# Performance work log

Hardware: AMD Instinct MI355X
Metric: run time of the kernel (lower is better)

The kernel has to match this reference:

```python
import jax, jax.numpy as jnp
import numpy as np

D_MODEL = 1024
NUM_HEADS = 16
D_K = D_MODEL // NUM_HEADS
ROPE_BASE = 10000.0


def _rotate_half(x):
    # interleaved pairs: (x0, x1) -> (-x1, x0)
    x1 = x[..., ::2]
    x2 = x[..., 1::2]
    return jnp.stack((-x2, x1), axis=-1).reshape(x.shape)


def _rope(q, k):
    seq_len = q.shape[-2]
    freqs = ROPE_BASE ** (jnp.arange(0, D_K, 2, dtype=q.dtype) / D_K)  # [D_K/2]
    angles = jnp.arange(seq_len, dtype=q.dtype)[:, None] / freqs[None, :]  # [S, D_K/2]
    sin = jnp.repeat(jnp.sin(angles), 2, axis=-1)[None, None]  # [1,1,S,D_K]
    cos = jnp.repeat(jnp.cos(angles), 2, axis=-1)[None, None]
    return q * cos + _rotate_half(q) * sin, k * cos + _rotate_half(k) * sin


def setup_inputs() -> dict:
    key = jax.random.key(0)
    ks = jax.random.split(key, 9)
    B, S, D = 2, 2048, D_MODEL
    s = 1.0 / np.sqrt(D)
    inp = {
        "x": jax.random.normal(ks[0], (B, S, D), dtype=jnp.float32),
        "wq": jax.random.uniform(ks[1], (D, D), jnp.float32, -s, s),
        "bq": jax.random.uniform(ks[2], (D,), jnp.float32, -s, s),
        "wk": jax.random.uniform(ks[3], (D, D), jnp.float32, -s, s),
        "bk": jax.random.uniform(ks[4], (D,), jnp.float32, -s, s),
        "wv": jax.random.uniform(ks[5], (D, D), jnp.float32, -s, s),
        "bv": jax.random.uniform(ks[6], (D,), jnp.float32, -s, s),
        "wo": jax.random.uniform(ks[7], (D, D), jnp.float32, -s, s),
        "bo": jax.random.uniform(ks[8], (D,), jnp.float32, -s, s),
    }
    return inp


def reference(x, wq, bq, wk, bk, wv, bv, wo, bo):
    B, S, D = x.shape
    H, dk = NUM_HEADS, D_K
    # torch Linear: y = x @ W.T + b
    Q = (x @ wq.T + bq).reshape(B, S, H, dk).transpose(0, 2, 1, 3)  # [B,H,S,dk]
    K = (x @ wk.T + bk).reshape(B, S, H, dk).transpose(0, 2, 1, 3)
    V = (x @ wv.T + bv).reshape(B, S, H, dk).transpose(0, 2, 1, 3)
    Q, K = _rope(Q, K)
    score = jnp.einsum("bhqd,bhkd->bhqk", Q, K) / jnp.sqrt(jnp.asarray(dk, x.dtype))
    attn_w = jax.nn.softmax(score, axis=-1)
    out = jnp.einsum("bhqk,bhkd->bhqd", attn_w, V)  # [B,H,S,dk]
    out = out.transpose(0, 2, 1, 3).reshape(B, S, D)
    return out @ wo.T + bo
```

## Files before the change

### kernel.cpp

```cpp
#include <hip/hip_runtime.h>
#include <hip/hip_bf16.h>
#include <math.h>

typedef __bf16 bf16_t;
typedef __bf16 bf16x4_t __attribute__((ext_vector_type(4)));
typedef __bf16 bf16x8_t __attribute__((ext_vector_type(8)));
typedef float  f32x4_t  __attribute__((ext_vector_type(4)));

#define SEQ 2048
#define DM  1024
#define NH  16
#define DK  64
#define ROPE_C 0.4152410118609203f
#define EXP_C (1.4426950408889634f / 8.0f)

#define GLD16(gp, lp) \
  __builtin_amdgcn_global_load_lds((__attribute__((address_space(1))) const void*)(gp), \
                                   (__attribute__((address_space(3))) void*)(lp), 16, 0, 0)

__global__ __launch_bounds__(256)
void prep_kernel(const float* __restrict__ x,  const float* __restrict__ wq,
                 const float* __restrict__ wk, const float* __restrict__ wv,
                 const float* __restrict__ wo, bf16_t* __restrict__ dst,
                 float2* __restrict__ lut) {
  if (blockIdx.x < 8192) {
    int i = blockIdx.x * 256 + threadIdx.x;
    const float* s;
    if (i < 1048576) {
      s = x + (size_t)i * 4;
    } else {
      int j = i - 1048576;
      int w = j >> 18;
      const float* base = (w == 0) ? wq : (w == 1) ? wk : (w == 2) ? wv : wo;
      s = base + (size_t)(j & 262143) * 4;
    }
    float4 v = *(const float4*)s;
    bf16x4_t o;
    o.x = (bf16_t)v.x; o.y = (bf16_t)v.y; o.z = (bf16_t)v.z; o.w = (bf16_t)v.w;
    ((bf16x4_t*)dst)[i] = o;
  } else {
    int i = (blockIdx.x - 8192) * 256 + threadIdx.x;
    int s = i >> 5, f = i & 31;
    float ang = (float)s * exp2f(-ROPE_C * (float)f);
    float sn, cs;
    sincosf(ang, &sn, &cs);
    lut[i] = make_float2(sn, cs);
  }
}

__global__ __launch_bounds__(256, 3)
void gemm_qkv(const bf16_t* __restrict__ A, const bf16_t* __restrict__ Wq,
              const bf16_t* __restrict__ Wk, const bf16_t* __restrict__ Wv,
              const float* __restrict__ bq, const float* __restrict__ bk,
              const float* __restrict__ bv, const float2* __restrict__ lut,
              bf16_t* __restrict__ Qb, bf16_t* __restrict__ Kb,
              bf16_t* __restrict__ Vtb) {
  const int K = 1024;
  __shared__ bf16_t As[128 * 64];
  __shared__ bf16_t Bs[128 * 64];

  const int tid  = threadIdx.x;
  const int w    = tid >> 6;
  const int lane = tid & 63;
  const int quad = lane >> 4;
  const int lrow = lane & 15;
  const int wm = (w >> 1) * 64, wn = (w & 1) * 64;

  const int srow8 = lane >> 3;
  const int scolz = (((lane & 7) ^ (lane >> 3)) * 8);

  const int id   = blockIdx.x;
  const int xcd  = id & 7;
  const int rank = id >> 3;
  const int isV  = rank >= 64;

  const bf16_t* Ablk;
  const bf16_t* Bblk;
  int bmQK = 0, bnl = 0, isK = 0, bmF = 0, bnT = 0;
  if (!isV) {
    const int q = xcd * 64 + rank;
    bmQK = q >> 4;
    const int bn = q & 15;
    isK = bn >> 3;
    bnl = bn & 7;
    Ablk = A + (size_t)(bmQK * 128) * K;
    Bblk = (isK ? Wk : Wq) + (size_t)(bnl * 128) * K;
  } else {
    const int v = xcd * 32 + (rank - 64);
    bnT = v >> 3;
    bmF = v & 7;
    Ablk = Wv + (size_t)(bmF * 128) * K;
    Bblk = A + (size_t)(bnT * 128) * K;
  }

  f32x4_t acc[4][4] = {};

  for (int k0 = 0; k0 < K; k0 += 64) {
#pragma unroll
    for (int i = 0; i < 4; i++) {
      GLD16(&Ablk[(size_t)(w * 32 + i * 8 + srow8) * K + k0 + scolz], &As[(w * 32 + i * 8) * 64]);
      GLD16(&Bblk[(size_t)(w * 32 + i * 8 + srow8) * K + k0 + scolz], &Bs[(w * 32 + i * 8) * 64]);
    }
    __syncthreads();

#pragma unroll
    for (int kk = 0; kk < 2; kk++) {
      const int gsw = (((kk << 2) | quad) ^ (lrow & 7)) * 8;
      bf16x8_t af[4], bf[4];
#pragma unroll
      for (int mi = 0; mi < 4; mi++)
        af[mi] = *(const bf16x8_t*)(&As[(wm + mi * 16 + lrow) * 64 + gsw]);
#pragma unroll
      for (int ni = 0; ni < 4; ni++)
        bf[ni] = *(const bf16x8_t*)(&Bs[(wn + ni * 16 + lrow) * 64 + gsw]);
#pragma unroll
      for (int mi = 0; mi < 4; mi++)
#pragma unroll
        for (int ni = 0; ni < 4; ni++)
          acc[mi][ni] = __builtin_amdgcn_mfma_f32_16x16x32_bf16(af[mi], bf[ni], acc[mi][ni], 0, 0, 0);
    }
    __syncthreads();
  }

  if (!isV) {
    const int brow = bmQK * 128 + wm;
    const int cbase = bnl * 128 + wn;
    const float* bias = isK ? bk : bq;
    bf16_t* D = isK ? Kb : Qb;

#pragma unroll
    for (int ni = 0; ni < 4; ni++) {
      const int col = cbase + ni * 16 + lrow;
      const float bvv = bias[col];
      const int t = col & 63;
      const int h = col >> 6;
      const int fidx = t >> 1;
#pragma unroll
      for (int mi = 0; mi < 4; mi++) {
        f32x4_t v = acc[mi][ni];
#pragma unroll
        for (int r = 0; r < 4; r++) {
          const int row = brow + mi * 16 + quad * 4 + r;
          const int s = row & (SEQ - 1);
          float val = v[r] + bvv;
          const float2 sc = lut[s * 32 + fidx];
          const float pv = __shfl_xor(val, 1);
          val = (t & 1) ? (val * sc.y + pv * sc.x) : (val * sc.y - pv * sc.x);
          const int b = row >> 11;
          const size_t o = (((size_t)(b * NH + h) * SEQ) + s) * DK + t;
          D[o] = (bf16_t)val;
        }
      }
    }
  } else {
    const int fbase = bmF * 128 + wm;
    const int tbase = bnT * 128 + wn;

#pragma unroll
    for (int ni = 0; ni < 4; ni++) {
      const int t = tbase + ni * 16 + lrow;
      const int b = t >> 11;
      const int s = t & (SEQ - 1);
#pragma unroll
      for (int mi = 0; mi < 4; mi++) {
        f32x4_t v = acc[mi][ni];
        const int f = fbase + mi * 16 + quad * 4;
        const int h = f >> 6, d = f & 63;
#pragma unroll
        for (int r = 0; r < 4; r++)
          Vtb[((size_t)((b * NH + h) * DK + d + r)) * SEQ + s] = (bf16_t)(v[r] + bv[f + r]);
      }
    }
  }
}

__global__ __launch_bounds__(256)
void gemm_out(const bf16_t* __restrict__ A, const bf16_t* __restrict__ Bw,
              const float* __restrict__ bias, float* __restrict__ D) {
  const int K = 1024;
  __shared__ bf16_t As[128 * 64];
  __shared__ bf16_t Bs[64 * 64];

  const int tid  = threadIdx.x;
  const int w    = tid >> 6;
  const int lane = tid & 63;
  const int quad = lane >> 4;
  const int lrow = lane & 15;
  const int wm = (w >> 1) * 64, wn = (w & 1) * 32;

  const int srow8 = lane >> 3;
  const int scolz = (((lane & 7) ^ (lane >> 3)) * 8);

  const int id  = blockIdx.x;
  const int swz = (id & 7) * 64 + (id >> 3);
  const int bm  = swz >> 4;
  const int bn  = swz & 15;

  const bf16_t* Ablk = A  + (size_t)(bm * 128) * K;
  const bf16_t* Bblk = Bw + (size_t)(bn * 64) * K;

  f32x4_t acc[4][2] = {};

  for (int k0 = 0; k0 < K; k0 += 64) {
#pragma unroll
    for (int i = 0; i < 4; i++)
      GLD16(&Ablk[(size_t)(w * 32 + i * 8 + srow8) * K + k0 + scolz], &As[(w * 32 + i * 8) * 64]);
#pragma unroll
    for (int i = 0; i < 2; i++)
      GLD16(&Bblk[(size_t)(w * 16 + i * 8 + srow8) * K + k0 + scolz], &Bs[(w * 16 + i * 8) * 64]);
    __syncthreads();

#pragma unroll
    for (int kk = 0; kk < 2; kk++) {
      const int gsw = (((kk << 2) | quad) ^ (lrow & 7)) * 8;
      bf16x8_t af[4], bf[2];
#pragma unroll
      for (int mi = 0; mi < 4; mi++)
        af[mi] = *(const bf16x8_t*)(&As[(wm + mi * 16 + lrow) * 64 + gsw]);
#pragma unroll
      for (int ni = 0; ni < 2; ni++)
        bf[ni] = *(const bf16x8_t*)(&Bs[(wn + ni * 16 + lrow) * 64 + gsw]);
#pragma unroll
      for (int mi = 0; mi < 4; mi++)
#pragma unroll
        for (int ni = 0; ni < 2; ni++)
          acc[mi][ni] = __builtin_amdgcn_mfma_f32_16x16x32_bf16(af[mi], bf[ni], acc[mi][ni], 0, 0, 0);
    }
    __syncthreads();
  }

#pragma unroll
  for (int ni = 0; ni < 2; ni++) {
    const int col = bn * 64 + wn + ni * 16 + lrow;
    const float bvv = bias[col];
#pragma unroll
    for (int mi = 0; mi < 4; mi++) {
      f32x4_t v = acc[mi][ni];
#pragma unroll
      for (int r = 0; r < 4; r++) {
        const int row = bm * 128 + wm + mi * 16 + quad * 4 + r;
        D[(size_t)row * DM + col] = v[r] + bvv;
      }
    }
  }
}

__global__ __launch_bounds__(256, 4)
void attn_kernel(const bf16_t* __restrict__ Q, const bf16_t* __restrict__ K,
                 const bf16_t* __restrict__ Vt, bf16_t* __restrict__ AO) {
  __shared__ bf16_t Ks[128 * 64];
  __shared__ bf16_t Vs[64 * 128];

  const int tid  = threadIdx.x;
  const int w    = tid >> 6;
  const int lane = tid & 63;
  const int quad = lane >> 4;
  const int lrow = lane & 15;

  const int id  = blockIdx.x;
  const int swz = (id & 7) * 128 + (id >> 3);
  const int bh  = swz >> 5;
  const int q0  = (swz & 31) * 64 + w * 16;

  const bf16_t* Qh  = Q  + (size_t)bh * SEQ * DK;
  const bf16_t* Kh  = K  + (size_t)bh * SEQ * DK;
  const bf16_t* Vth = Vt + (size_t)bh * DK * SEQ;

  bf16x8_t qf[2];
#pragma unroll
  for (int c = 0; c < 2; c++) {
    bf16x8_t t = *(const bf16x8_t*)(&Qh[(size_t)(q0 + lrow) * DK + c * 32 + quad * 8]);
#pragma unroll
    for (int i = 0; i < 8; i++) t[i] = (bf16_t)((float)t[i] * EXP_C);
    qf[c] = t;
  }

  f32x4_t accO[4] = {};
  float lsum = 0.f;

  const int krow = tid >> 1;
  const int kcol = (tid & 1) * 32;
  const int kg0  = (tid & 1) * 4;
  const int ksw  = krow & 7;
  const int kwr  = krow * 64;
  const int kw0 = kwr + (((kg0 + 0) ^ ksw) << 3);
  const int kw1 = kwr + (((kg0 + 1) ^ ksw) << 3);
  const int kw2 = kwr + (((kg0 + 2) ^ ksw) << 3);
  const int kw3 = kwr + (((kg0 + 3) ^ ksw) << 3);

  const int vrow = tid >> 2;
  const int vcol = (tid & 3) * 32;
  const int vG   = (tid & 3) * 4;
  const int vsw  = vrow & 15;
  const int vwr  = vrow * 128;
  const int vw0 = vwr + (((vG + 0) ^ vsw) << 3);
  const int vw1 = vwr + (((vG + 1) ^ vsw) << 3);
  const int vw2 = vwr + (((vG + 2) ^ vsw) << 3);
  const int vw3 = vwr + (((vG + 3) ^ vsw) << 3);

  uint4 kr0 = *(const uint4*)(&Kh[(size_t)krow * DK + kcol]);
  uint4 kr1 = *(const uint4*)(&Kh[(size_t)krow * DK + kcol + 8]);
  uint4 kr2 = *(const uint4*)(&Kh[(size_t)krow * DK + kcol + 16]);
  uint4 kr3 = *(const uint4*)(&Kh[(size_t)krow * DK + kcol + 24]);
  uint4 vr0 = *(const uint4*)(&Vth[(size_t)vrow * SEQ + vcol]);
  uint4 vr1 = *(const uint4*)(&Vth[(size_t)vrow * SEQ + vcol + 8]);
  uint4 vr2 = *(const uint4*)(&Vth[(size_t)vrow * SEQ + vcol + 16]);
  uint4 vr3 = *(const uint4*)(&Vth[(size_t)vrow * SEQ + vcol + 24]);

  for (int kt = 0; kt < SEQ / 128; ++kt) {
    *(uint4*)(&Ks[kw0]) = kr0;
    *(uint4*)(&Ks[kw1]) = kr1;
    *(uint4*)(&Ks[kw2]) = kr2;
    *(uint4*)(&Ks[kw3]) = kr3;
    *(uint2*)(&Vs[vw0])     = make_uint2(vr0.x, vr0.y);
    *(uint2*)(&Vs[vw1])     = make_uint2(vr0.z, vr0.w);
    *(uint2*)(&Vs[vw2])     = make_uint2(vr1.x, vr1.y);
    *(uint2*)(&Vs[vw3])     = make_uint2(vr1.z, vr1.w);
    *(uint2*)(&Vs[vw0 + 4]) = make_uint2(vr2.x, vr2.y);
    *(uint2*)(&Vs[vw1 + 4]) = make_uint2(vr2.z, vr2.w);
    *(uint2*)(&Vs[vw2 + 4]) = make_uint2(vr3.x, vr3.y);
    *(uint2*)(&Vs[vw3 + 4]) = make_uint2(vr3.z, vr3.w);
    __syncthreads();

    if (kt + 1 < SEQ / 128) {
      const int kb = (kt + 1) * 128;
      kr0 = *(const uint4*)(&Kh[(size_t)(kb + krow) * DK + kcol]);
      kr1 = *(const uint4*)(&Kh[(size_t)(kb + krow) * DK + kcol + 8]);
      kr2 = *(const uint4*)(&Kh[(size_t)(kb + krow) * DK + kcol + 16]);
      kr3 = *(const uint4*)(&Kh[(size_t)(kb + krow) * DK + kcol + 24]);
      vr0 = *(const uint4*)(&Vth[(size_t)vrow * SEQ + kb + vcol]);
      vr1 = *(const uint4*)(&Vth[(size_t)vrow * SEQ + kb + vcol + 8]);
      vr2 = *(const uint4*)(&Vth[(size_t)vrow * SEQ + kb + vcol + 16]);
      vr3 = *(const uint4*)(&Vth[(size_t)vrow * SEQ + kb + vcol + 24]);
    }

    __builtin_amdgcn_s_setprio(1);
#pragma unroll
    for (int c2 = 0; c2 < 4; ++c2) {
      uint2 pk[2];
#pragma unroll
      for (int kk2 = 0; kk2 < 2; ++kk2) {
        const int kk = c2 * 2 + kk2;
        const int krd = (kk * 16 + lrow) * 64;
        bf16x8_t kf0 = *(const bf16x8_t*)(&Ks[krd + ((quad       ^ (lrow & 7)) << 3)]);
        bf16x8_t kf1 = *(const bf16x8_t*)(&Ks[krd + (((quad + 4) ^ (lrow & 7)) << 3)]);
        f32x4_t z = {};
        z = __builtin_amdgcn_mfma_f32_16x16x32_bf16(kf0, qf[0], z, 0, 0, 0);
        z = __builtin_amdgcn_mfma_f32_16x16x32_bf16(kf1, qf[1], z, 0, 0, 0);
        const float p0 = __builtin_amdgcn_exp2f(z[0]), p1 = __builtin_amdgcn_exp2f(z[1]);
        const float p2 = __builtin_amdgcn_exp2f(z[2]), p3 = __builtin_amdgcn_exp2f(z[3]);
        lsum += (p0 + p1) + (p2 + p3);
        pk[kk2].x = __builtin_amdgcn_perm(__builtin_bit_cast(unsigned, p1),
                                          __builtin_bit_cast(unsigned, p0), 0x07060302u);
        pk[kk2].y = __builtin_amdgcn_perm(__builtin_bit_cast(unsigned, p3),
                                          __builtin_bit_cast(unsigned, p2), 0x07060302u);
      }
      uint4 pfu;
      pfu.x = pk[0].x; pfu.y = pk[0].y; pfu.z = pk[1].x; pfu.w = pk[1].y;
      bf16x8_t pf = __builtin_bit_cast(bf16x8_t, pfu);
#pragma unroll
      for (int nt = 0; nt < 4; ++nt) {
        bf16x8_t vf = *(const bf16x8_t*)(
            &Vs[(nt * 16 + lrow) * 128 + ((((c2 << 2) | quad) ^ lrow) << 3)]);
        accO[nt] = __builtin_amdgcn_mfma_f32_16x16x32_bf16(pf, vf, accO[nt], 0, 0, 0);
      }
    }
    __builtin_amdgcn_s_setprio(0);
    __syncthreads();
  }

  lsum += __shfl_xor(lsum, 16);
  lsum += __shfl_xor(lsum, 32);
  float linv[4];
#pragma unroll
  for (int r = 0; r < 4; r++)
    linv[r] = 1.0f / __shfl(lsum, quad * 4 + r);

  const int b = bh >> 4, h = bh & 15;
#pragma unroll
  for (int nt = 0; nt < 4; nt++)
#pragma unroll
    for (int r = 0; r < 4; r++) {
      const int srowq = q0 + quad * 4 + r;
      const float val = accO[nt][r] * linv[r];
      const size_t o = ((size_t)(b * SEQ + srowq)) * DM + h * DK + nt * 16 + lrow;
      AO[o] = (bf16_t)val;
    }
}

extern "C" void kernel_launch(void* const* d_in, const int* in_sizes, int n_in,
                              void* d_out, int out_size, void* d_ws, size_t ws_size,
                              hipStream_t stream) {
  const float* x  = (const float*)d_in[0];
  const float* wq = (const float*)d_in[1];
  const float* bq = (const float*)d_in[2];
  const float* wk = (const float*)d_in[3];
  const float* bk = (const float*)d_in[4];
  const float* wv = (const float*)d_in[5];
  const float* bv = (const float*)d_in[6];
  const float* wo = (const float*)d_in[7];
  const float* bo = (const float*)d_in[8];
  float* out = (float*)d_out;

  char* ws = (char*)d_ws;
  bf16_t* xb   = (bf16_t*)(ws);
  bf16_t* wqb  = (bf16_t*)(ws + 8388608);
  bf16_t* wkb  = (bf16_t*)(ws + 10485760);
  bf16_t* wvb  = (bf16_t*)(ws + 12582912);
  bf16_t* wob  = (bf16_t*)(ws + 14680064);
  bf16_t* Qb   = (bf16_t*)(ws + 16777216);
  bf16_t* Kb   = (bf16_t*)(ws + 25165824);
  bf16_t* Vtb  = (bf16_t*)(ws + 33554432);
  bf16_t* AOb  = (bf16_t*)(ws + 41943040);
  float2* lut  = (float2*)(ws + 50331648);

  prep_kernel<<<8448, 256, 0, stream>>>(x, wq, wk, wv, wo, xb, lut);

  gemm_qkv<<<768, 256, 0, stream>>>(xb, wqb, wkb, wvb, bq, bk, bv, lut, Qb, Kb, Vtb);

  attn_kernel<<<1024, 256, 0, stream>>>(Qb, Kb, Vtb, AOb);

  gemm_out<<<512, 256, 0, stream>>>(AOb, wob, bo, out);
}
```

Baseline: 183.4 us.

## Process two 16-row query tiles per wave in attention to reuse K/V fragments

Each wave now handles 32 query rows, as two 16-row tiles, instead of 16. Each K and V fragment read from LDS feeds two MFMAs, and each block covers 128 query rows, so the grid halves to 512 blocks. This halves K/V global loads and LDS staging per query row. In exchange it raises register pressure (launch bounds drop to 2 blocks per SM), which lowers occupancy and leaves fewer blocks to balance across CUs.

```diff
diff --git a/kernel.cpp b/kernel.cpp
--- a/kernel.cpp
+++ b/kernel.cpp
@@ -245,7 +245,7 @@
   }
 }
 
-__global__ __launch_bounds__(256, 4)
+__global__ __launch_bounds__(256, 2)
 void attn_kernel(const bf16_t* __restrict__ Q, const bf16_t* __restrict__ K,
                  const bf16_t* __restrict__ Vt, bf16_t* __restrict__ AO) {
   __shared__ bf16_t Ks[128 * 64];
@@ -258,25 +258,29 @@
   const int lrow = lane & 15;
 
   const int id  = blockIdx.x;
-  const int swz = (id & 7) * 128 + (id >> 3);
-  const int bh  = swz >> 5;
-  const int q0  = (swz & 31) * 64 + w * 16;
+  const int swz = (id & 7) * 64 + (id >> 3);
+  const int bh  = swz >> 4;
+  const int q0  = (swz & 15) * 128 + w * 32;
 
   const bf16_t* Qh  = Q  + (size_t)bh * SEQ * DK;
   const bf16_t* Kh  = K  + (size_t)bh * SEQ * DK;
   const bf16_t* Vth = Vt + (size_t)bh * DK * SEQ;
 
-  bf16x8_t qf[2];
+  bf16x8_t qfA[2], qfB[2];
 #pragma unroll
   for (int c = 0; c < 2; c++) {
-    bf16x8_t t = *(const bf16x8_t*)(&Qh[(size_t)(q0 + lrow) * DK + c * 32 + quad * 8]);
-#pragma unroll
-    for (int i = 0; i < 8; i++) t[i] = (bf16_t)((float)t[i] * EXP_C);
-    qf[c] = t;
-  }
-
-  f32x4_t accO[4] = {};
-  float lsum = 0.f;
+    bf16x8_t ta = *(const bf16x8_t*)(&Qh[(size_t)(q0 + lrow) * DK + c * 32 + quad * 8]);
+    bf16x8_t tb = *(const bf16x8_t*)(&Qh[(size_t)(q0 + 16 + lrow) * DK + c * 32 + quad * 8]);
+#pragma unroll
+    for (int i = 0; i < 8; i++) {
+      ta[i] = (bf16_t)((float)ta[i] * EXP_C);
+      tb[i] = (bf16_t)((float)tb[i] * EXP_C);
+    }
+    qfA[c] = ta; qfB[c] = tb;
+  }
+
+  f32x4_t accA[4] = {}, accB[4] = {};
+  float lsumA = 0.f, lsumB = 0.f;
 
   const int krow = tid >> 1;
   const int kcol = (tid & 1) * 32;
@@ -337,54 +341,72 @@
     __builtin_amdgcn_s_setprio(1);
 #pragma unroll
     for (int c2 = 0; c2 < 4; ++c2) {
-      uint2 pk[2];
+      uint2 pkA[2], pkB[2];
 #pragma unroll
       for (int kk2 = 0; kk2 < 2; ++kk2) {
         const int kk = c2 * 2 + kk2;
         const int krd = (kk * 16 + lrow) * 64;
         bf16x8_t kf0 = *(const bf16x8_t*)(&Ks[krd + ((quad       ^ (lrow & 7)) << 3)]);
         bf16x8_t kf1 = *(const bf16x8_t*)(&Ks[krd + (((quad + 4) ^ (lrow & 7)) << 3)]);
-        f32x4_t z = {};
-        z = __builtin_amdgcn_mfma_f32_16x16x32_bf16(kf0, qf[0], z, 0, 0, 0);
-        z = __builtin_amdgcn_mfma_f32_16x16x32_bf16(kf1, qf[1], z, 0, 0, 0);
-        const float p0 = __builtin_amdgcn_exp2f(z[0]), p1 = __builtin_amdgcn_exp2f(z[1]);
-        const float p2 = __builtin_amdgcn_exp2f(z[2]), p3 = __builtin_amdgcn_exp2f(z[3]);
-        lsum += (p0 + p1) + (p2 + p3);
-        pk[kk2].x = __builtin_amdgcn_perm(__builtin_bit_cast(unsigned, p1),
-                                          __builtin_bit_cast(unsigned, p0), 0x07060302u);
-        pk[kk2].y = __builtin_amdgcn_perm(__builtin_bit_cast(unsigned, p3),
-                                          __builtin_bit_cast(unsigned, p2), 0x07060302u);
+        f32x4_t zA = {}, zB = {};
+        zA = __builtin_amdgcn_mfma_f32_16x16x32_bf16(kf0, qfA[0], zA, 0, 0, 0);
+        zA = __builtin_amdgcn_mfma_f32_16x16x32_bf16(kf1, qfA[1], zA, 0, 0, 0);
+        zB = __builtin_amdgcn_mfma_f32_16x16x32_bf16(kf0, qfB[0], zB, 0, 0, 0);
+        zB = __builtin_amdgcn_mfma_f32_16x16x32_bf16(kf1, qfB[1], zB, 0, 0, 0);
+        const float a0 = __builtin_amdgcn_exp2f(zA[0]), a1 = __builtin_amdgcn_exp2f(zA[1]);
+        const float a2 = __builtin_amdgcn_exp2f(zA[2]), a3 = __builtin_amdgcn_exp2f(zA[3]);
+        const float b0 = __builtin_amdgcn_exp2f(zB[0]), b1 = __builtin_amdgcn_exp2f(zB[1]);
+        const float b2 = __builtin_amdgcn_exp2f(zB[2]), b3 = __builtin_amdgcn_exp2f(zB[3]);
+        lsumA += (a0 + a1) + (a2 + a3);
+        lsumB += (b0 + b1) + (b2 + b3);
+        pkA[kk2].x = __builtin_amdgcn_perm(__builtin_bit_cast(unsigned, a1),
+                                           __builtin_bit_cast(unsigned, a0), 0x07060302u);
+        pkA[kk2].y = __builtin_amdgcn_perm(__builtin_bit_cast(unsigned, a3),
+                                           __builtin_bit_cast(unsigned, a2), 0x07060302u);
+        pkB[kk2].x = __builtin_amdgcn_perm(__builtin_bit_cast(unsigned, b1),
+                                           __builtin_bit_cast(unsigned, b0), 0x07060302u);
+        pkB[kk2].y = __builtin_amdgcn_perm(__builtin_bit_cast(unsigned, b3),
+                                           __builtin_bit_cast(unsigned, b2), 0x07060302u);
       }
-      uint4 pfu;
-      pfu.x = pk[0].x; pfu.y = pk[0].y; pfu.z = pk[1].x; pfu.w = pk[1].y;
-      bf16x8_t pf = __builtin_bit_cast(bf16x8_t, pfu);
+      uint4 pfuA, pfuB;
+      pfuA.x = pkA[0].x; pfuA.y = pkA[0].y; pfuA.z = pkA[1].x; pfuA.w = pkA[1].y;
+      pfuB.x = pkB[0].x; pfuB.y = pkB[0].y; pfuB.z = pkB[1].x; pfuB.w = pkB[1].y;
+      bf16x8_t pfA = __builtin_bit_cast(bf16x8_t, pfuA);
+      bf16x8_t pfB = __builtin_bit_cast(bf16x8_t, pfuB);
 #pragma unroll
       for (int nt = 0; nt < 4; ++nt) {
         bf16x8_t vf = *(const bf16x8_t*)(
             &Vs[(nt * 16 + lrow) * 128 + ((((c2 << 2) | quad) ^ lrow) << 3)]);
-        accO[nt] = __builtin_amdgcn_mfma_f32_16x16x32_bf16(pf, vf, accO[nt], 0, 0, 0);
+        accA[nt] = __builtin_amdgcn_mfma_f32_16x16x32_bf16(pfA, vf, accA[nt], 0, 0, 0);
+        accB[nt] = __builtin_amdgcn_mfma_f32_16x16x32_bf16(pfB, vf, accB[nt], 0, 0, 0);
       }
     }
     __builtin_amdgcn_s_setprio(0);
     __syncthreads();
   }
 
-  lsum += __shfl_xor(lsum, 16);
-  lsum += __shfl_xor(lsum, 32);
-  float linv[4];
-#pragma unroll
-  for (int r = 0; r < 4; r++)
-    linv[r] = 1.0f / __shfl(lsum, quad * 4 + r);
+  lsumA += __shfl_xor(lsumA, 16);
+  lsumA += __shfl_xor(lsumA, 32);
+  lsumB += __shfl_xor(lsumB, 16);
+  lsumB += __shfl_xor(lsumB, 32);
+  float linvA[4], linvB[4];
+#pragma unroll
+  for (int r = 0; r < 4; r++) {
+    linvA[r] = 1.0f / __shfl(lsumA, quad * 4 + r);
+    linvB[r] = 1.0f / __shfl(lsumB, quad * 4 + r);
+  }
 
   const int b = bh >> 4, h = bh & 15;
 #pragma unroll
   for (int nt = 0; nt < 4; nt++)
 #pragma unroll
     for (int r = 0; r < 4; r++) {
-      const int srowq = q0 + quad * 4 + r;
-      const float val = accO[nt][r] * linv[r];
-      const size_t o = ((size_t)(b * SEQ + srowq)) * DM + h * DK + nt * 16 + lrow;
-      AO[o] = (bf16_t)val;
+      const int rowA = q0 + quad * 4 + r;
+      const int rowB = q0 + 16 + quad * 4 + r;
+      const float va = accA[nt][r] * linvA[r];
+      const float vb = accB[nt][r] * linvB[r];
+      AO[((size_t)(b * SEQ + rowA)) * DM + h * DK + nt * 16 + lrow] = (bf16_t)va;
+      AO[((size_t)(b * SEQ + rowB)) * DM + h * DK + nt * 16 + lrow] = (bf16_t)vb;
     }
 }
 
@@ -418,7 +440,7 @@
 
   gemm_qkv<<<768, 256, 0, stream>>>(xb, wqb, wkb, wvb, bq, bk, bv, lut, Qb, Kb, Vtb);
 
-  attn_kernel<<<1024, 256, 0, stream>>>(Qb, Kb, Vtb, AOb);
+  attn_kernel<<<512, 256, 0, stream>>>(Qb, Kb, Vtb, AOb);
 
   gemm_out<<<512, 256, 0, stream>>>(AOb, wob, bo, out);
 }
```

Result: faster. 171.7 us, median of 3 (-6.4%).
